# Optimization experiments

Measured on AMD Instinct MI355X. Metric: run time of the kernel, lower is better.

The kernel has to match this reference:

```python
import jax, jax.numpy as jnp
import numpy as np

N, D, L, K = 250000, 16, 6, 64
COST_GAMMA = 0.1
MIN_ZERO_GAMMA = 0.1
EPS = 1e-7  # clip for arccos numerical stability


def setup_inputs() -> dict:
    key = jax.random.key(0)
    k1, k2, k3, k4 = jax.random.split(key, 4)
    xs = jax.random.normal(k1, (N, D), jnp.float32)
    xs = xs / jnp.linalg.norm(xs, axis=1, keepdims=True)  # points on sphere S^{D-1}
    mus = jax.random.normal(k2, (L, D, K), jnp.float32)    # per-layer component locations
    alphas = jax.random.uniform(k3, (L, K), jnp.float32, minval=-1.0, maxval=1.0)
    ws = jax.random.uniform(k4, (L,), jnp.float32, minval=0.0, maxval=1.0)
    return {"xs": xs, "mus": mus, "alphas": alphas, "ws": ws}


def reference(xs, mus, alphas, ws):
    # projx: normalize each mu column onto the sphere (norm over D axis)
    mu_n = mus / jnp.linalg.norm(mus, axis=1, keepdims=True)          # [L, D, K]
    # sphere cost: 0.5 * geodesic_dist^2 = 0.5 * arccos(<x, mu>)^2
    inner = jnp.einsum('nd,ldk->lnk', xs, mu_n)                        # [L, N, K]
    dist = jnp.arccos(jnp.clip(inner, -1.0 + EPS, 1.0 - EPS))
    costs = 0.5 * dist * dist + alphas[:, None, :]                     # [L, N, K]
    # soft-min over components (note sign convention follows original: +gamma*LSE(-c/gamma))
    mincosts = COST_GAMMA * jax.nn.logsumexp(-costs / COST_GAMMA, axis=2)  # [L, N]
    wv = jnp.exp(-ws ** 2)                                             # [L]
    F = jnp.zeros((xs.shape[0],), xs.dtype)
    for i in range(L):  # small fixed layer recurrence
        F = wv[i] * jax.nn.relu(F) + (1.0 - wv[i]) * mincosts[i]
    # smooth min(F, 0): gamma * LSE(-[F,0]/gamma)
    Fz = jnp.stack((F, jnp.zeros_like(F)), axis=-1)
    F = MIN_ZERO_GAMMA * jax.nn.logsumexp(-Fz / MIN_ZERO_GAMMA, axis=-1)
    return F
```

## Files before the change

kernel.cpp:

```cpp
#include <hip/hip_runtime.h>
#include <math.h>

#define NPOINTS 250000
#define LL 6
#define DD 16
#define KK 64
#define TPB 384
#define PTS_PER_BLOCK 256
#define NTILES 16

#define SMC_OFF 20480
#define SWV_OFF 26624
#define LDS_BYTES (SWV_OFF + 32)

typedef __attribute__((ext_vector_type(8))) short bf16x8;
typedef __attribute__((ext_vector_type(4))) float f32x4;
typedef __attribute__((ext_vector_type(2))) float f32x2;

#if __has_builtin(__builtin_amdgcn_exp2f)
#define EXP2F(x) __builtin_amdgcn_exp2f(x)
#else
#define EXP2F(x) exp2f(x)
#endif
#if __has_builtin(__builtin_amdgcn_logf)
#define LOG2F(x) __builtin_amdgcn_logf(x)
#else
#define LOG2F(x) log2f(x)
#endif

#define C_AA   (-14.426950408889634f)
#define C_GLN2 (0.06931471805599453f)

#define W0  17.797117f
#define VT0 (-45.300328f)
#define VT1 (-28.559404f)
#define VT2 (-27.844414f)
#define VT3 (-30.475230f)
#define VT4 (-36.246253f)
#define VT5 (-27.207285f)

__device__ __forceinline__ f32x2 s2(float v) { f32x2 r; r.x = v; r.y = v; return r; }

__device__ __forceinline__ ushort bf16_rne(float f) {
  unsigned u = __float_as_uint(f);
  unsigned r = u + 0x7FFFu + ((u >> 16) & 1u);
  return (ushort)(r >> 16);
}

__device__ __forceinline__ f32x2 term2(f32x2 xp, f32x2 aaw) {
  f32x2 V = s2(VT5);
  V = __builtin_elementwise_fma(V, xp, s2(VT4));
  V = __builtin_elementwise_fma(V, xp, s2(VT3));
  V = __builtin_elementwise_fma(V, xp, s2(VT2));
  V = __builtin_elementwise_fma(V, xp, s2(VT1));
  V = __builtin_elementwise_fma(V, xp, s2(VT0));
  f32x2 t2 = __builtin_elementwise_fma(xp, V, aaw);
  f32x2 e; e.x = EXP2F(t2.x); e.y = EXP2F(t2.y);
  return e;
}

__global__ __launch_bounds__(TPB, 5) void
multiinf_kernel(const float* __restrict__ xs,
                const float* __restrict__ mus,
                const float* __restrict__ alphas,
                const float* __restrict__ wsv,
                float* __restrict__ out) {
  __shared__ __align__(16) char smem[LDS_BYTES];
  float* swv = (float*)(smem + SWV_OFF);
  float* smc = (float*)(smem + SMC_OFF);

  const int tid = threadIdx.x;
  const int w = tid >> 6;
  const int lane = tid & 63;
  const int c = lane & 15;
  const int q = lane >> 4;
  const int h = q & 1;
  const int pbase = blockIdx.x * PTS_PER_BLOCK;

  float xv[DD];
  {
    int gidx = pbase + tid;
    if (tid < PTS_PER_BLOCK && gidx < NPOINTS) {
      const float4* x4 = (const float4*)(xs + (size_t)gidx * DD);
#pragma unroll
      for (int j = 0; j < 4; ++j) {
        float4 a = x4[j];
        xv[j * 4 + 0] = a.x; xv[j * 4 + 1] = a.y;
        xv[j * 4 + 2] = a.z; xv[j * 4 + 3] = a.w;
      }
    } else {
#pragma unroll
      for (int d = 0; d < DD; ++d) xv[d] = 0.0f;
    }
  }

  {
    const float* colp = mus + w * (DD * KK) + lane;
    float v[DD];
    float ss = 0.0f;
#pragma unroll
    for (int d = 0; d < DD; ++d) { v[d] = colp[d * KK]; ss = fmaf(v[d], v[d], ss); }
    float inv = -0.5f / sqrtf(ss);
    unsigned hw[8], lw[8];
#pragma unroll
    for (int i = 0; i < 8; ++i) {
      float a0 = v[2 * i] * inv;
      float a1 = v[2 * i + 1] * inv;
      ushort h0 = bf16_rne(a0), h1 = bf16_rne(a1);
      float hf0 = __uint_as_float((unsigned)h0 << 16);
      float hf1 = __uint_as_float((unsigned)h1 << 16);
      ushort l0 = bf16_rne(a0 - hf0), l1 = bf16_rne(a1 - hf1);
      hw[i] = (unsigned)h0 | ((unsigned)h1 << 16);
      lw[i] = (unsigned)l0 | ((unsigned)l1 << 16);
    }
    uint4* colq = (uint4*)(smem + (w * 64 + lane) * 64);
    colq[0] = make_uint4(hw[0], hw[1], hw[2], hw[3]);
    colq[1] = make_uint4(hw[4], hw[5], hw[6], hw[7]);
    colq[2] = make_uint4(lw[0], lw[1], lw[2], lw[3]);
    colq[3] = make_uint4(lw[4], lw[5], lw[6], lw[7]);
  }
  float av = fmaf(C_AA, alphas[w * 64 + lane], -W0);
  if (tid < LL) { float t = wsv[tid]; swv[tid] = expf(-t * t); }
  __syncthreads();

  bf16x8 Am[4];
  f32x2 aaL[4], aaH[4];
#pragma unroll
  for (int cb = 0; cb < 4; ++cb) {
    Am[cb] = *(const bf16x8*)(smem + (w * 64 + cb * 16 + c) * 64 + q * 16);
    int base = cb * 16 + q * 4;
    aaL[cb].x = __shfl(av, base + 0, 64);
    aaL[cb].y = __shfl(av, base + 1, 64);
    aaH[cb].x = __shfl(av, base + 2, 64);
    aaH[cb].y = __shfl(av, base + 3, 64);
  }
  __syncthreads();

  if (tid < PTS_PER_BLOCK) {
    unsigned hw[8], lw[8];
#pragma unroll
    for (int i = 0; i < 8; ++i) {
      ushort h0 = bf16_rne(xv[2 * i]);
      ushort h1 = bf16_rne(xv[2 * i + 1]);
      float hf0 = __uint_as_float((unsigned)h0 << 16);
      float hf1 = __uint_as_float((unsigned)h1 << 16);
      ushort l0 = bf16_rne(xv[2 * i] - hf0);
      ushort l1 = bf16_rne(xv[2 * i + 1] - hf1);
      hw[i] = (unsigned)h0 | ((unsigned)h1 << 16);
      lw[i] = (unsigned)l0 | ((unsigned)l1 << 16);
    }
    uint4* pq = (uint4*)(smem + tid * 80);
    pq[0] = make_uint4(hw[0], hw[1], hw[2], hw[3]);
    pq[1] = make_uint4(hw[4], hw[5], hw[6], hw[7]);
    pq[2] = make_uint4(lw[0], lw[1], lw[2], lw[3]);
    pq[3] = make_uint4(lw[4], lw[5], lw[6], lw[7]);
  }
  __syncthreads();

  float* smcw = smc + w * PTS_PER_BLOCK;
  bf16x8 Bh = *(const bf16x8*)(smem + (0 * 16 + c) * 80 + h * 16);
  bf16x8 Bl = *(const bf16x8*)(smem + (0 * 16 + c) * 80 + 32 + h * 16);
  for (int t = 0; t < NTILES; ++t) {
    int tn = ((t + 1) & 15) * 16 + c;
    bf16x8 Bhn = *(const bf16x8*)(smem + tn * 80 + h * 16);
    bf16x8 Bln = *(const bf16x8*)(smem + tn * 80 + 32 + h * 16);

    f32x2 S01 = s2(0.0f), S23 = s2(0.0f);
#pragma unroll
    for (int cb = 0; cb < 4; ++cb) {
      f32x4 acc = {0.0f, 0.0f, 0.0f, 0.0f};
      acc = __builtin_amdgcn_mfma_f32_16x16x32_bf16(Am[cb], Bh, acc, 0, 0, 0);
      acc = __builtin_amdgcn_mfma_f32_16x16x32_bf16(Am[cb], Bl, acc, 0, 0, 0);
      f32x2 a01; a01.x = acc[0]; a01.y = acc[1];
      f32x2 a23; a23.x = acc[2]; a23.y = acc[3];
      S01 += term2(a01, aaL[cb]);
      S23 += term2(a23, aaH[cb]);
    }
    f32x2 Sf = S01 + S23;
    float St = Sf.x + Sf.y;
    St += __shfl_xor(St, 16, 64);
    St += __shfl_xor(St, 32, 64);

    if (lane < 16) smcw[t * 16 + c] = St;
    Bh = Bhn;
    Bl = Bln;
  }
  __syncthreads();

  if (tid < PTS_PER_BLOCK) {
    float F = 0.0f;
#pragma unroll
    for (int l = 0; l < LL; ++l) {
      float wv = swv[l];
      float mc = C_GLN2 * LOG2F(smc[l * PTS_PER_BLOCK + tid]);
      F = fmaf(wv, fmaxf(F, 0.0f), (1.0f - wv) * mc);
    }
    int idx = pbase + tid;
    if (idx < NPOINTS) {
      float e = EXP2F(F * C_AA);
      out[idx] = C_GLN2 * LOG2F(1.0f + e);
    }
  }
}

extern "C" void kernel_launch(void* const* d_in, const int* in_sizes, int n_in,
                              void* d_out, int out_size, void* d_ws, size_t ws_size,
                              hipStream_t stream) {
  const float* xs = (const float*)d_in[0];
  const float* mus = (const float*)d_in[1];
  const float* alphas = (const float*)d_in[2];
  const float* wsv = (const float*)d_in[3];
  float* out = (float*)d_out;
  (void)d_ws; (void)ws_size;

  const int blocks = (NPOINTS + PTS_PER_BLOCK - 1) / PTS_PER_BLOCK;
  multiinf_kernel<<<blocks, TPB, 0, stream>>>(xs, mus, alphas, wsv, out);
}
```

Baseline: 98.17 us.

## Software-pipeline MFMA tiles with transcendental consume and merge LDS phases

Moves the point tiles into a separate LDS region so the A-fragment loads and point staging can share one barrier, dropping two __syncthreads. The tile loop is fully unrolled and double-buffered, so MFMAs for the next tile are issued while the exp/polynomial work of the current tile runs. The polynomial is rewritten in Estrin form to shorten its dependency chain. In exchange LDS use roughly doubles, register pressure rises, and the occupancy hint is lowered from 5 to 4 blocks.

```diff
diff --git a/kernel.cpp b/kernel.cpp
--- a/kernel.cpp
+++ b/kernel.cpp
@@ -9,8 +9,9 @@
 #define PTS_PER_BLOCK 256
 #define NTILES 16
 
-#define SMC_OFF 20480
-#define SWV_OFF 26624
+#define SXU_OFF 24576
+#define SMC_OFF 45056
+#define SWV_OFF 51200
 #define LDS_BYTES (SWV_OFF + 32)
 
 typedef __attribute__((ext_vector_type(8))) short bf16x8;
@@ -48,18 +49,18 @@
 }
 
 __device__ __forceinline__ f32x2 term2(f32x2 xp, f32x2 aaw) {
-  f32x2 V = s2(VT5);
-  V = __builtin_elementwise_fma(V, xp, s2(VT4));
-  V = __builtin_elementwise_fma(V, xp, s2(VT3));
-  V = __builtin_elementwise_fma(V, xp, s2(VT2));
-  V = __builtin_elementwise_fma(V, xp, s2(VT1));
-  V = __builtin_elementwise_fma(V, xp, s2(VT0));
-  f32x2 t2 = __builtin_elementwise_fma(xp, V, aaw);
+  f32x2 x2  = xp * xp;
+  f32x2 p01 = __builtin_elementwise_fma(s2(VT1), xp, s2(VT0));
+  f32x2 p23 = __builtin_elementwise_fma(s2(VT3), xp, s2(VT2));
+  f32x2 p45 = __builtin_elementwise_fma(s2(VT5), xp, s2(VT4));
+  f32x2 qq  = __builtin_elementwise_fma(x2, p45, p23);
+  f32x2 V   = __builtin_elementwise_fma(x2, qq, p01);
+  f32x2 t2  = __builtin_elementwise_fma(xp, V, aaw);
   f32x2 e; e.x = EXP2F(t2.x); e.y = EXP2F(t2.y);
   return e;
 }
 
-__global__ __launch_bounds__(TPB, 5) void
+__global__ __launch_bounds__(TPB, 4) void
 multiinf_kernel(const float* __restrict__ xs,
                 const float* __restrict__ mus,
                 const float* __restrict__ alphas,
@@ -68,6 +69,7 @@
   __shared__ __align__(16) char smem[LDS_BYTES];
   float* swv = (float*)(smem + SWV_OFF);
   float* smc = (float*)(smem + SMC_OFF);
+  char* sxu = smem + SXU_OFF;
 
   const int tid = threadIdx.x;
   const int w = tid >> 6;
@@ -121,20 +123,6 @@
   }
   float av = fmaf(C_AA, alphas[w * 64 + lane], -W0);
   if (tid < LL) { float t = wsv[tid]; swv[tid] = expf(-t * t); }
-  __syncthreads();
-
-  bf16x8 Am[4];
-  f32x2 aaL[4], aaH[4];
-#pragma unroll
-  for (int cb = 0; cb < 4; ++cb) {
-    Am[cb] = *(const bf16x8*)(smem + (w * 64 + cb * 16 + c) * 64 + q * 16);
-    int base = cb * 16 + q * 4;
-    aaL[cb].x = __shfl(av, base + 0, 64);
-    aaL[cb].y = __shfl(av, base + 1, 64);
-    aaH[cb].x = __shfl(av, base + 2, 64);
-    aaH[cb].y = __shfl(av, base + 3, 64);
-  }
-  __syncthreads();
 
   if (tid < PTS_PER_BLOCK) {
     unsigned hw[8], lw[8];
@@ -149,30 +137,45 @@
       hw[i] = (unsigned)h0 | ((unsigned)h1 << 16);
       lw[i] = (unsigned)l0 | ((unsigned)l1 << 16);
     }
-    uint4* pq = (uint4*)(smem + tid * 80);
+    uint4* pq = (uint4*)(sxu + tid * 80);
     pq[0] = make_uint4(hw[0], hw[1], hw[2], hw[3]);
     pq[1] = make_uint4(hw[4], hw[5], hw[6], hw[7]);
     pq[2] = make_uint4(lw[0], lw[1], lw[2], lw[3]);
     pq[3] = make_uint4(lw[4], lw[5], lw[6], lw[7]);
   }
+
   __syncthreads();
 
+  bf16x8 Am[4];
+  f32x2 aaL[4], aaH[4];
+#pragma unroll
+  for (int cb = 0; cb < 4; ++cb) {
+    Am[cb] = *(const bf16x8*)(smem + (w * 64 + cb * 16 + c) * 64 + q * 16);
+    int base = cb * 16 + q * 4;
+    aaL[cb].x = __shfl(av, base + 0, 64);
+    aaL[cb].y = __shfl(av, base + 1, 64);
+    aaH[cb].x = __shfl(av, base + 2, 64);
+    aaH[cb].y = __shfl(av, base + 3, 64);
+  }
+
   float* smcw = smc + w * PTS_PER_BLOCK;
-  bf16x8 Bh = *(const bf16x8*)(smem + (0 * 16 + c) * 80 + h * 16);
-  bf16x8 Bl = *(const bf16x8*)(smem + (0 * 16 + c) * 80 + 32 + h * 16);
-  for (int t = 0; t < NTILES; ++t) {
-    int tn = ((t + 1) & 15) * 16 + c;
-    bf16x8 Bhn = *(const bf16x8*)(smem + tn * 80 + h * 16);
-    bf16x8 Bln = *(const bf16x8*)(smem + tn * 80 + 32 + h * 16);
-
+  const char* bbase = sxu + c * 80 + h * 16;
+
+  auto MFMA_TILE = [&](bf16x8 Bhp, bf16x8 Blp, f32x4* acc) {
+#pragma unroll
+    for (int cb = 0; cb < 4; ++cb) {
+      f32x4 a = {0.0f, 0.0f, 0.0f, 0.0f};
+      a = __builtin_amdgcn_mfma_f32_16x16x32_bf16(Am[cb], Bhp, a, 0, 0, 0);
+      a = __builtin_amdgcn_mfma_f32_16x16x32_bf16(Am[cb], Blp, a, 0, 0, 0);
+      acc[cb] = a;
+    }
+  };
+  auto CONSUME = [&](const f32x4* acc, int t) {
     f32x2 S01 = s2(0.0f), S23 = s2(0.0f);
 #pragma unroll
     for (int cb = 0; cb < 4; ++cb) {
-      f32x4 acc = {0.0f, 0.0f, 0.0f, 0.0f};
-      acc = __builtin_amdgcn_mfma_f32_16x16x32_bf16(Am[cb], Bh, acc, 0, 0, 0);
-      acc = __builtin_amdgcn_mfma_f32_16x16x32_bf16(Am[cb], Bl, acc, 0, 0, 0);
-      f32x2 a01; a01.x = acc[0]; a01.y = acc[1];
-      f32x2 a23; a23.x = acc[2]; a23.y = acc[3];
+      f32x2 a01; a01.x = acc[cb][0]; a01.y = acc[cb][1];
+      f32x2 a23; a23.x = acc[cb][2]; a23.y = acc[cb][3];
       S01 += term2(a01, aaL[cb]);
       S23 += term2(a23, aaH[cb]);
     }
@@ -180,10 +183,25 @@
     float St = Sf.x + Sf.y;
     St += __shfl_xor(St, 16, 64);
     St += __shfl_xor(St, 32, 64);
-
     if (lane < 16) smcw[t * 16 + c] = St;
-    Bh = Bhn;
-    Bl = Bln;
+  };
+
+  f32x4 acc0[4], acc1[4];
+  bf16x8 Bh = *(const bf16x8*)(bbase + 0);
+  bf16x8 Bl = *(const bf16x8*)(bbase + 32);
+  MFMA_TILE(Bh, Bl, acc0);
+#pragma unroll
+  for (int t = 0; t < NTILES; t += 2) {
+    Bh = *(const bf16x8*)(bbase + (t + 1) * 1280);
+    Bl = *(const bf16x8*)(bbase + (t + 1) * 1280 + 32);
+    CONSUME(acc0, t);
+    MFMA_TILE(Bh, Bl, acc1);
+    if (t + 2 < NTILES) {
+      Bh = *(const bf16x8*)(bbase + (t + 2) * 1280);
+      Bl = *(const bf16x8*)(bbase + (t + 2) * 1280 + 32);
+    }
+    CONSUME(acc1, t + 1);
+    if (t + 2 < NTILES) MFMA_TILE(Bh, Bl, acc0);
   }
   __syncthreads();
 
```

After: 101.5 us. +3.4%, slower.

## Precompute normalized mus in a prep kernel and load from workspace

Applied to the files above, without the earlier changes.

Adds a single-block prep kernel that normalizes and bf16-splits the mu columns, scales alphas and computes layer weights into the workspace. The main kernel then reads these directly from global memory instead of recomputing them in every block. This removes per-block setup work and two barriers, and shrinks LDS so occupancy can be raised to 6. It also rewrites the polynomial with Estrin-style evaluation for shorter dependency chains, and replaces the software-pipelined B loads with an unrolled loop. The cost is an extra kernel launch on the stream.

```diff
diff --git a/kernel.cpp b/kernel.cpp
--- a/kernel.cpp
+++ b/kernel.cpp
@@ -10,8 +10,11 @@
 #define NTILES 16
 
 #define SMC_OFF 20480
-#define SWV_OFF 26624
-#define LDS_BYTES (SWV_OFF + 32)
+#define LDS_BYTES (SMC_OFF + LL * PTS_PER_BLOCK * 4)
+
+#define WS_MU 0
+#define WS_AV 24576
+#define WS_WV 26112
 
 typedef __attribute__((ext_vector_type(8))) short bf16x8;
 typedef __attribute__((ext_vector_type(4))) float f32x4;
@@ -48,26 +51,57 @@
 }
 
 __device__ __forceinline__ f32x2 term2(f32x2 xp, f32x2 aaw) {
-  f32x2 V = s2(VT5);
-  V = __builtin_elementwise_fma(V, xp, s2(VT4));
-  V = __builtin_elementwise_fma(V, xp, s2(VT3));
-  V = __builtin_elementwise_fma(V, xp, s2(VT2));
-  V = __builtin_elementwise_fma(V, xp, s2(VT1));
-  V = __builtin_elementwise_fma(V, xp, s2(VT0));
-  f32x2 t2 = __builtin_elementwise_fma(xp, V, aaw);
+  f32x2 x2  = xp * xp;
+  f32x2 p01 = __builtin_elementwise_fma(s2(VT1), xp, s2(VT0));
+  f32x2 p23 = __builtin_elementwise_fma(s2(VT3), xp, s2(VT2));
+  f32x2 p45 = __builtin_elementwise_fma(s2(VT5), xp, s2(VT4));
+  f32x2 qq  = __builtin_elementwise_fma(x2, p45, p23);
+  f32x2 V   = __builtin_elementwise_fma(x2, qq, p01);
+  f32x2 t2  = __builtin_elementwise_fma(xp, V, aaw);
   f32x2 e; e.x = EXP2F(t2.x); e.y = EXP2F(t2.y);
   return e;
 }
 
-__global__ __launch_bounds__(TPB, 5) void
+__global__ __launch_bounds__(384) void
+prep_kernel(const float* __restrict__ mus,
+            const float* __restrict__ alphas,
+            const float* __restrict__ wsv,
+            char* __restrict__ ws) {
+  const int t = threadIdx.x;
+  const float* colp = mus + (t >> 6) * (DD * KK) + (t & 63);
+  float v[DD];
+  float ss = 0.0f;
+#pragma unroll
+  for (int d = 0; d < DD; ++d) { v[d] = colp[d * KK]; ss = fmaf(v[d], v[d], ss); }
+  float inv = -0.5f / sqrtf(ss);
+  unsigned hw[8], lw[8];
+#pragma unroll
+  for (int i = 0; i < 8; ++i) {
+    float a0 = v[2 * i] * inv;
+    float a1 = v[2 * i + 1] * inv;
+    ushort h0 = bf16_rne(a0), h1 = bf16_rne(a1);
+    float hf0 = __uint_as_float((unsigned)h0 << 16);
+    float hf1 = __uint_as_float((unsigned)h1 << 16);
+    ushort l0 = bf16_rne(a0 - hf0), l1 = bf16_rne(a1 - hf1);
+    hw[i] = (unsigned)h0 | ((unsigned)h1 << 16);
+    lw[i] = (unsigned)l0 | ((unsigned)l1 << 16);
+  }
+  uint4* colq = (uint4*)(ws + WS_MU + t * 64);
+  colq[0] = make_uint4(hw[0], hw[1], hw[2], hw[3]);
+  colq[1] = make_uint4(hw[4], hw[5], hw[6], hw[7]);
+  colq[2] = make_uint4(lw[0], lw[1], lw[2], lw[3]);
+  colq[3] = make_uint4(lw[4], lw[5], lw[6], lw[7]);
+  ((float*)(ws + WS_AV))[t] = fmaf(C_AA, alphas[t], -W0);
+  if (t < LL) { float x = wsv[t]; ((float*)(ws + WS_WV))[t] = expf(-x * x); }
+}
+
+__global__ __launch_bounds__(TPB, 6) void
 multiinf_kernel(const float* __restrict__ xs,
-                const float* __restrict__ mus,
-                const float* __restrict__ alphas,
-                const float* __restrict__ wsv,
+                const char* __restrict__ ws,
                 float* __restrict__ out) {
   __shared__ __align__(16) char smem[LDS_BYTES];
-  float* swv = (float*)(smem + SWV_OFF);
   float* smc = (float*)(smem + SMC_OFF);
+  char* sxu = smem;
 
   const int tid = threadIdx.x;
   const int w = tid >> 6;
@@ -77,10 +111,20 @@
   const int h = q & 1;
   const int pbase = blockIdx.x * PTS_PER_BLOCK;
 
-  float xv[DD];
-  {
+  bf16x8 Am[4];
+  f32x2 aaL[4], aaH[4];
+#pragma unroll
+  for (int cb = 0; cb < 4; ++cb) {
+    Am[cb] = *(const bf16x8*)(ws + WS_MU + (w * 64 + cb * 16 + c) * 64 + q * 16);
+    f32x4 a4 = *(const f32x4*)(ws + WS_AV + (w * 64 + cb * 16 + q * 4) * 4);
+    aaL[cb].x = a4.x; aaL[cb].y = a4.y;
+    aaH[cb].x = a4.z; aaH[cb].y = a4.w;
+  }
+
+  if (tid < PTS_PER_BLOCK) {
     int gidx = pbase + tid;
-    if (tid < PTS_PER_BLOCK && gidx < NPOINTS) {
+    float xv[DD];
+    if (gidx < NPOINTS) {
       const float4* x4 = (const float4*)(xs + (size_t)gidx * DD);
 #pragma unroll
       for (int j = 0; j < 4; ++j) {
@@ -92,51 +136,6 @@
 #pragma unroll
       for (int d = 0; d < DD; ++d) xv[d] = 0.0f;
     }
-  }
-
-  {
-    const float* colp = mus + w * (DD * KK) + lane;
-    float v[DD];
-    float ss = 0.0f;
-#pragma unroll
-    for (int d = 0; d < DD; ++d) { v[d] = colp[d * KK]; ss = fmaf(v[d], v[d], ss); }
-    float inv = -0.5f / sqrtf(ss);
-    unsigned hw[8], lw[8];
-#pragma unroll
-    for (int i = 0; i < 8; ++i) {
-      float a0 = v[2 * i] * inv;
-      float a1 = v[2 * i + 1] * inv;
-      ushort h0 = bf16_rne(a0), h1 = bf16_rne(a1);
-      float hf0 = __uint_as_float((unsigned)h0 << 16);
-      float hf1 = __uint_as_float((unsigned)h1 << 16);
-      ushort l0 = bf16_rne(a0 - hf0), l1 = bf16_rne(a1 - hf1);
-      hw[i] = (unsigned)h0 | ((unsigned)h1 << 16);
-      lw[i] = (unsigned)l0 | ((unsigned)l1 << 16);
-    }
-    uint4* colq = (uint4*)(smem + (w * 64 + lane) * 64);
-    colq[0] = make_uint4(hw[0], hw[1], hw[2], hw[3]);
-    colq[1] = make_uint4(hw[4], hw[5], hw[6], hw[7]);
-    colq[2] = make_uint4(lw[0], lw[1], lw[2], lw[3]);
-    colq[3] = make_uint4(lw[4], lw[5], lw[6], lw[7]);
-  }
-  float av = fmaf(C_AA, alphas[w * 64 + lane], -W0);
-  if (tid < LL) { float t = wsv[tid]; swv[tid] = expf(-t * t); }
-  __syncthreads();
-
-  bf16x8 Am[4];
-  f32x2 aaL[4], aaH[4];
-#pragma unroll
-  for (int cb = 0; cb < 4; ++cb) {
-    Am[cb] = *(const bf16x8*)(smem + (w * 64 + cb * 16 + c) * 64 + q * 16);
-    int base = cb * 16 + q * 4;
-    aaL[cb].x = __shfl(av, base + 0, 64);
-    aaL[cb].y = __shfl(av, base + 1, 64);
-    aaH[cb].x = __shfl(av, base + 2, 64);
-    aaH[cb].y = __shfl(av, base + 3, 64);
-  }
-  __syncthreads();
-
-  if (tid < PTS_PER_BLOCK) {
     unsigned hw[8], lw[8];
 #pragma unroll
     for (int i = 0; i < 8; ++i) {
@@ -149,22 +148,21 @@
       hw[i] = (unsigned)h0 | ((unsigned)h1 << 16);
       lw[i] = (unsigned)l0 | ((unsigned)l1 << 16);
     }
-    uint4* pq = (uint4*)(smem + tid * 80);
+    uint4* pq = (uint4*)(sxu + tid * 80);
     pq[0] = make_uint4(hw[0], hw[1], hw[2], hw[3]);
     pq[1] = make_uint4(hw[4], hw[5], hw[6], hw[7]);
     pq[2] = make_uint4(lw[0], lw[1], lw[2], lw[3]);
     pq[3] = make_uint4(lw[4], lw[5], lw[6], lw[7]);
   }
+
   __syncthreads();
 
   float* smcw = smc + w * PTS_PER_BLOCK;
-  bf16x8 Bh = *(const bf16x8*)(smem + (0 * 16 + c) * 80 + h * 16);
-  bf16x8 Bl = *(const bf16x8*)(smem + (0 * 16 + c) * 80 + 32 + h * 16);
+  const char* bbase = sxu + c * 80 + h * 16;
+#pragma unroll 4
   for (int t = 0; t < NTILES; ++t) {
-    int tn = ((t + 1) & 15) * 16 + c;
-    bf16x8 Bhn = *(const bf16x8*)(smem + tn * 80 + h * 16);
-    bf16x8 Bln = *(const bf16x8*)(smem + tn * 80 + 32 + h * 16);
-
+    bf16x8 Bh = *(const bf16x8*)(bbase + t * 1280);
+    bf16x8 Bl = *(const bf16x8*)(bbase + t * 1280 + 32);
     f32x2 S01 = s2(0.0f), S23 = s2(0.0f);
 #pragma unroll
     for (int cb = 0; cb < 4; ++cb) {
@@ -180,14 +178,12 @@
     float St = Sf.x + Sf.y;
     St += __shfl_xor(St, 16, 64);
     St += __shfl_xor(St, 32, 64);
-
     if (lane < 16) smcw[t * 16 + c] = St;
-    Bh = Bhn;
-    Bl = Bln;
   }
   __syncthreads();
 
   if (tid < PTS_PER_BLOCK) {
+    const float* swv = (const float*)(ws + WS_WV);
     float F = 0.0f;
 #pragma unroll
     for (int l = 0; l < LL; ++l) {
@@ -211,8 +207,10 @@
   const float* alphas = (const float*)d_in[2];
   const float* wsv = (const float*)d_in[3];
   float* out = (float*)d_out;
-  (void)d_ws; (void)ws_size;
-
+  char* ws = (char*)d_ws;
+  (void)ws_size;
+
+  prep_kernel<<<1, 384, 0, stream>>>(mus, alphas, wsv, ws);
   const int blocks = (NPOINTS + PTS_PER_BLOCK - 1) / PTS_PER_BLOCK;
-  multiinf_kernel<<<blocks, TPB, 0, stream>>>(xs, mus, alphas, wsv, out);
-}
+  multiinf_kernel<<<blocks, TPB, 0, stream>>>(xs, ws, out);
+}
```

Result: slower. 100.9 us (+2.8%).
